# Kernel optimization log

Measured on AMD Instinct MI355X. Metric: run time of the kernel, lower is better.

The kernel has to match this reference:

```python
import jax, jax.numpy as jnp
import numpy as np

N_NODES = 100000
N_EDGES = 1600000
N_GRAPHS = 512
HIDDEN = 128
N_LAYERS = 3


def setup_inputs() -> dict:
    key = jax.random.key(0)
    ks = jax.random.split(key, 16)
    X = jax.random.normal(ks[0], (N_NODES, HIDDEN), dtype=jnp.float32)
    edge_index = jax.random.randint(ks[1], (2, N_EDGES), 0, N_NODES, dtype=jnp.int64)
    batch = jnp.sort(jax.random.randint(ks[2], (N_NODES,), 0, N_GRAPHS, dtype=jnp.int64))
    s = 1.0 / np.sqrt(HIDDEN)
    mlp_w1 = jax.random.normal(ks[3], (N_LAYERS, HIDDEN, HIDDEN), dtype=jnp.float32) * s
    mlp_b1 = jnp.zeros((N_LAYERS, HIDDEN), dtype=jnp.float32)
    mlp_w2 = jax.random.normal(ks[4], (N_LAYERS, HIDDEN, HIDDEN), dtype=jnp.float32) * s
    mlp_b2 = jnp.zeros((N_LAYERS, HIDDEN), dtype=jnp.float32)
    cls_w1 = jax.random.normal(ks[5], (HIDDEN * N_LAYERS, HIDDEN), dtype=jnp.float32) / np.sqrt(HIDDEN * N_LAYERS)
    cls_b1 = jnp.zeros((HIDDEN,), dtype=jnp.float32)
    cls_w2 = jax.random.normal(ks[6], (HIDDEN, HIDDEN), dtype=jnp.float32) * s
    cls_b2 = jnp.zeros((HIDDEN,), dtype=jnp.float32)
    cls_w3 = jax.random.normal(ks[7], (HIDDEN, 1), dtype=jnp.float32) * s
    cls_b3 = jnp.zeros((1,), dtype=jnp.float32)
    return {"X": X, "edge_index": edge_index, "batch": batch,
            "mlp_w1": mlp_w1, "mlp_b1": mlp_b1, "mlp_w2": mlp_w2, "mlp_b2": mlp_b2,
            "cls_w1": cls_w1, "cls_b1": cls_b1, "cls_w2": cls_w2, "cls_b2": cls_b2,
            "cls_w3": cls_w3, "cls_b3": cls_b3}


def reference(X, edge_index, batch, mlp_w1, mlp_b1, mlp_w2, mlp_b2,
              cls_w1, cls_b1, cls_w2, cls_b2, cls_w3, cls_b3):
    src, dst = edge_index[0], edge_index[1]
    xs = []
    for l in range(N_LAYERS):
        # GIN aggregation: sum_{j in N(i)} x_j ; eps = 0 so add self feature
        agg = jax.ops.segment_sum(X[src], dst, num_segments=N_NODES)  # [N, H]
        z = X + agg
        # 2-layer MLP update
        h = jax.nn.relu(z @ mlp_w1[l] + mlp_b1[l])
        h = h @ mlp_w2[l] + mlp_b2[l]
        # dropout is identity in eval; then relu
        X = jax.nn.relu(h)
        # global sum pooling per graph
        xs.append(jax.ops.segment_sum(X, batch, num_segments=N_GRAPHS))  # [G, H]
    h = jnp.concatenate(xs, axis=-1)  # JK 'cat' -> [G, H*L]
    h = jax.nn.relu(h @ cls_w1 + cls_b1)
    h = jax.nn.relu(h @ cls_w2 + cls_b2)
    logits = h @ cls_w3 + cls_b3  # [G, 1]
    return logits
```

## Files before the change

kernel.cpp:

```cpp
#include <hip/hip_runtime.h>
#include <hip/hip_fp16.h>
#include <cstddef>
#include <cstdint>

#define N_NODES   100000
#define N_EDGES   1600000
#define N_GRAPHS  512
#define HIDDEN    128
#define N_LAYERS  3

#define N_WIN        400
#define WIN_NODES    (N_NODES / N_WIN)
#define PLACE_BLOCKS 128
#define PCHUNK       (N_EDGES / PLACE_BLOCKS)

#define F2H_BLOCKS   ((N_NODES * HIDDEN / 8) / 256)
#define WCONV_BLOCKS (N_LAYERS * 2 * 16)
#define GB_BLOCKS    2
#define PREP_BLOCKS  (F2H_BLOCKS + WCONV_BLOCKS + GB_BLOCKS)

typedef _Float16 half8  __attribute__((ext_vector_type(8)));
typedef _Float16 half4v __attribute__((ext_vector_type(4)));
typedef _Float16 half2v __attribute__((ext_vector_type(2)));
typedef float    float8 __attribute__((ext_vector_type(8)));
typedef float    floatx4 __attribute__((ext_vector_type(4)));
typedef float    floatx2 __attribute__((ext_vector_type(2)));

__global__ __launch_bounds__(256) void win_count_kernel(const int* __restrict__ dst,
                                                        int* __restrict__ counts) {
    __shared__ int cs[N_WIN];
    for (int i = threadIdx.x; i < N_WIN; i += 256) cs[i] = 0;
    __syncthreads();
    const int4* d4 = (const int4*)(dst + blockIdx.x * PCHUNK);
    for (int i = threadIdx.x; i < PCHUNK / 4; i += 256) {
        int4 d = d4[i];
        atomicAdd(&cs[d.x / WIN_NODES], 1);
        atomicAdd(&cs[d.y / WIN_NODES], 1);
        atomicAdd(&cs[d.z / WIN_NODES], 1);
        atomicAdd(&cs[d.w / WIN_NODES], 1);
    }
    __syncthreads();
    for (int i = threadIdx.x; i < N_WIN; i += 256)
        counts[blockIdx.x * N_WIN + i] = cs[i];
}

__global__ __launch_bounds__(128) void win_scan1_kernel(const int* __restrict__ counts,
                                                        int* __restrict__ offsets,
                                                        int* __restrict__ colsum) {
    __shared__ int tmp[128];
    const int w = blockIdx.x;
    const int t = threadIdx.x;
    tmp[t] = counts[t * N_WIN + w];
    __syncthreads();
#pragma unroll
    for (int off = 1; off < 128; off <<= 1) {
        int u = (t >= off) ? tmp[t - off] : 0;
        __syncthreads();
        tmp[t] += u;
        __syncthreads();
    }
    offsets[t * N_WIN + w] = (t == 0) ? 0 : tmp[t - 1];
    if (t == 127) colsum[w] = tmp[127];
}

__global__ __launch_bounds__(512) void win_place_kernel(const int* __restrict__ src,
                                                        const int* __restrict__ dst,
                                                        const int* __restrict__ offsets,
                                                        const int* __restrict__ colsum,
                                                        int2* __restrict__ wedge) {
    __shared__ int ws[512];
    __shared__ int off[N_WIN];
    const int t = threadIdx.x;
    ws[t] = (t < N_WIN) ? colsum[t] : 0;
    __syncthreads();
#pragma unroll
    for (int o = 1; o < 512; o <<= 1) {
        int u = (t >= o) ? ws[t - o] : 0;
        __syncthreads();
        ws[t] += u;
        __syncthreads();
    }
    if (t < N_WIN) off[t] = offsets[blockIdx.x * N_WIN + t] + ((t == 0) ? 0 : ws[t - 1]);
    __syncthreads();
    const int4* d4 = (const int4*)(dst + blockIdx.x * PCHUNK);
    const int4* s4 = (const int4*)(src + blockIdx.x * PCHUNK);
    for (int i = t; i < PCHUNK / 4; i += 512) {
        int4 d = d4[i];
        int4 s = s4[i];
        int p0 = atomicAdd(&off[d.x / WIN_NODES], 1); wedge[p0] = make_int2(d.x, s.x);
        int p1 = atomicAdd(&off[d.y / WIN_NODES], 1); wedge[p1] = make_int2(d.y, s.y);
        int p2 = atomicAdd(&off[d.z / WIN_NODES], 1); wedge[p2] = make_int2(d.z, s.z);
        int p3 = atomicAdd(&off[d.w / WIN_NODES], 1); wedge[p3] = make_int2(d.w, s.w);
    }
}

__global__ __launch_bounds__(512) void win_csr_kernel(const int2* __restrict__ wedge,
                                                      const int* __restrict__ colsum,
                                                      int* __restrict__ row_ptr,
                                                      int* __restrict__ csr_src) {
    __shared__ int ws[512];
    __shared__ int cnt[WIN_NODES];
    __shared__ int bb[2];
    const int w = blockIdx.x, n0 = w * WIN_NODES, t = threadIdx.x;
    ws[t] = (t < N_WIN) ? colsum[t] : 0;
    __syncthreads();
#pragma unroll
    for (int o = 1; o < 512; o <<= 1) {
        int u = (t >= o) ? ws[t - o] : 0;
        __syncthreads();
        ws[t] += u;
        __syncthreads();
    }
    if (t == 0) { bb[0] = (w > 0) ? ws[w - 1] : 0; bb[1] = ws[w]; }
    if (w == N_WIN - 1 && t == 0) row_ptr[N_NODES] = ws[N_WIN - 1];
    for (int i = t; i < WIN_NODES; i += 512) cnt[i] = 0;
    __syncthreads();
    const int b0 = bb[0], b1 = bb[1];
    for (int e = b0 + t; e < b1; e += 512)
        atomicAdd(&cnt[wedge[e].x - n0], 1);
    __syncthreads();
    ws[t] = (t < WIN_NODES) ? cnt[t] : 0;
    __syncthreads();
#pragma unroll
    for (int o = 1; o < 512; o <<= 1) {
        int u = (t >= o) ? ws[t - o] : 0;
        __syncthreads();
        ws[t] += u;
        __syncthreads();
    }
    const int excl = (t == 0) ? 0 : ws[t - 1];
    if (t < WIN_NODES) {
        row_ptr[n0 + t] = b0 + excl;
        cnt[t] = b0 + excl;
    }
    __syncthreads();
    for (int e = b0 + t; e < b1; e += 512) {
        int2 ed = wedge[e];
        int p = atomicAdd(&cnt[ed.x - n0], 1);
        csr_src[p] = ed.y;
    }
}

__global__ __launch_bounds__(256) void prep_kernel(const float* __restrict__ X,
                                                   __half* __restrict__ hA,
                                                   unsigned char* __restrict__ outq,
                                                   const float* __restrict__ w1,
                                                   const float* __restrict__ w2,
                                                   __half* __restrict__ wt1,
                                                   __half* __restrict__ wt2,
                                                   const int* __restrict__ batch,
                                                   int* __restrict__ gstart) {
    __shared__ float tile[32][33];
    const int b = blockIdx.x;
    if (b < F2H_BLOCKS) {
        int t = b * 256 + threadIdx.x;
        const float4* in4 = (const float4*)X;
        float4 a = in4[t * 2 + 0];
        float4 c = in4[t * 2 + 1];
        __half2* o2 = (__half2*)hA;
        o2[t * 4 + 0] = __floats2half2_rn(a.x, a.y);
        o2[t * 4 + 1] = __floats2half2_rn(a.z, a.w);
        o2[t * 4 + 2] = __floats2half2_rn(c.x, c.y);
        o2[t * 4 + 3] = __floats2half2_rn(c.z, c.w);
        unsigned r0 = 0, r1 = 0;
        r0 = __builtin_amdgcn_cvt_pk_fp8_f32(a.x, a.y, r0, false);
        r0 = __builtin_amdgcn_cvt_pk_fp8_f32(a.z, a.w, r0, true);
        r1 = __builtin_amdgcn_cvt_pk_fp8_f32(c.x, c.y, r1, false);
        r1 = __builtin_amdgcn_cvt_pk_fp8_f32(c.z, c.w, r1, true);
        ((uint2*)outq)[t] = make_uint2(r0, r1);
    } else if (b < F2H_BLOCKS + WCONV_BLOCKS) {
        const int bb = b - F2H_BLOCKS;
        const int mat = bb & 1;
        const int tt = (bb >> 1) & 15;
        const int l  = bb >> 5;
        const int ti = (tt >> 2) * 32, tj = (tt & 3) * 32;
        const float* W = (mat ? w2 : w1) + (size_t)l * HIDDEN * HIDDEN;
        __half* WT = (mat ? wt2 : wt1) + (size_t)l * HIDDEN * HIDDEN;
        const int r = threadIdx.x >> 5;
        const int c = threadIdx.x & 31;
#pragma unroll
        for (int rr = 0; rr < 4; ++rr)
            tile[r + 8 * rr][c] = W[(size_t)(ti + r + 8 * rr) * HIDDEN + tj + c];
        __syncthreads();
#pragma unroll
        for (int rr = 0; rr < 4; ++rr)
            WT[(size_t)(tj + r + 8 * rr) * HIDDEN + ti + c] =
                __float2half(tile[c][r + 8 * rr]);
    } else {
        const int g = (b - F2H_BLOCKS - WCONV_BLOCKS) * 256 + threadIdx.x;
        if (g < N_GRAPHS) {
            int lo = 0, hi = N_NODES;
            while (lo < hi) {
                int mid = (lo + hi) >> 1;
                if (batch[mid] < g) lo = mid + 1; else hi = mid;
            }
            gstart[g] = lo;
        }
        if (g == 0) gstart[N_GRAPHS] = N_NODES;
    }
}

__device__ __forceinline__ void acc_fp8x16(float* acc, uint4 v) {
    floatx2 f;
    f = __builtin_amdgcn_cvt_pk_f32_fp8(v.x, false); acc[0] += f.x;  acc[1] += f.y;
    f = __builtin_amdgcn_cvt_pk_f32_fp8(v.x, true);  acc[2] += f.x;  acc[3] += f.y;
    f = __builtin_amdgcn_cvt_pk_f32_fp8(v.y, false); acc[4] += f.x;  acc[5] += f.y;
    f = __builtin_amdgcn_cvt_pk_f32_fp8(v.y, true);  acc[6] += f.x;  acc[7] += f.y;
    f = __builtin_amdgcn_cvt_pk_f32_fp8(v.z, false); acc[8] += f.x;  acc[9] += f.y;
    f = __builtin_amdgcn_cvt_pk_f32_fp8(v.z, true);  acc[10] += f.x; acc[11] += f.y;
    f = __builtin_amdgcn_cvt_pk_f32_fp8(v.w, false); acc[12] += f.x; acc[13] += f.y;
    f = __builtin_amdgcn_cvt_pk_f32_fp8(v.w, true);  acc[14] += f.x; acc[15] += f.y;
}

__global__ void gather_kernel(const unsigned char* __restrict__ Xq,
                              const __half* __restrict__ Xh,
                              __half* __restrict__ Zh,
                              const int* __restrict__ row_ptr,
                              const int* __restrict__ csr_src) {
    int wave = (blockIdx.x * blockDim.x + threadIdx.x) >> 6;
    int lane = threadIdx.x & 63;
    if (wave >= N_NODES) return;
    const int grp = lane >> 3;
    const int m   = lane & 7;
    const uint4* Q = (const uint4*)Xq;

    float acc[16];
#pragma unroll
    for (int j = 0; j < 16; ++j) acc[j] = 0.f;

    int k = row_ptr[wave];
    const int end = row_ptr[wave + 1];

    for (; k + 16 <= end; k += 16) {
        int n0 = csr_src[k + grp];
        int n1 = csr_src[k + 8 + grp];
        uint4 v0 = Q[(size_t)n0 * 8 + m];
        uint4 v1 = Q[(size_t)n1 * 8 + m];
        acc_fp8x16(acc, v0);
        acc_fp8x16(acc, v1);
    }
    if (k + 8 <= end) {
        int n0 = csr_src[k + grp];
        uint4 v0 = Q[(size_t)n0 * 8 + m];
        acc_fp8x16(acc, v0);
        k += 8;
    }
    int rem = end - k;
    if (grp < rem) {
        int n0 = csr_src[k + grp];
        uint4 v0 = Q[(size_t)n0 * 8 + m];
        acc_fp8x16(acc, v0);
    }

    half2v hh[8];
#pragma unroll
    for (int j = 0; j < 8; ++j) {
        hh[j][0] = (_Float16)acc[2 * j];
        hh[j][1] = (_Float16)acc[2 * j + 1];
    }
#pragma unroll
    for (int j = 0; j < 8; ++j) {
        int b = __shfl_xor(__builtin_bit_cast(int, hh[j]), 8);
        hh[j] = hh[j] + __builtin_bit_cast(half2v, b);
    }
#pragma unroll
    for (int j = 0; j < 8; ++j) {
        int b = __shfl_xor(__builtin_bit_cast(int, hh[j]), 16);
        hh[j] = hh[j] + __builtin_bit_cast(half2v, b);
    }
#pragma unroll
    for (int j = 0; j < 8; ++j) {
        int b = __shfl_xor(__builtin_bit_cast(int, hh[j]), 32);
        hh[j] = hh[j] + __builtin_bit_cast(half2v, b);
    }

    if (grp == 0) {
        const half2v* H2 = (const half2v*)(Xh + (size_t)wave * HIDDEN + 16 * m);
        half8 o0, o1;
#pragma unroll
        for (int j = 0; j < 4; ++j) {
            half2v s = hh[j] + H2[j];
            o0[2 * j] = s[0]; o0[2 * j + 1] = s[1];
        }
#pragma unroll
        for (int j = 0; j < 4; ++j) {
            half2v s = hh[4 + j] + H2[4 + j];
            o1[2 * j] = s[0]; o1[2 * j + 1] = s[1];
        }
        ((half8*)(Zh + (size_t)wave * HIDDEN + 16 * m))[0] = o0;
        ((half8*)(Zh + (size_t)wave * HIDDEN + 16 * m))[1] = o1;
    }
}

#define MM_BLOCKS 512
__global__ __launch_bounds__(256, 2) void mm_stage_kernel(const __half* __restrict__ A,
                                                          const __half* __restrict__ Wt,
                                                          const float* __restrict__ bias,
                                                          __half* __restrict__ C16,
                                                          unsigned char* __restrict__ Q8) {
    const int gwave = (blockIdx.x * 256 + threadIdx.x) >> 6;
    const int lane  = threadIdx.x & 63;
    const int m = lane & 15;
    const int q = lane >> 4;
    const int nwaves = MM_BLOCKS * 4;
    const int NTILES = N_NODES / 16;

    half8 wf[8][4];
    float bl[8][4];
#pragma unroll
    for (int ct = 0; ct < 8; ++ct) {
        const half8* Wrow = (const half8*)(Wt + (size_t)(ct * 16 + m) * HIDDEN);
#pragma unroll
        for (int c = 0; c < 4; ++c) wf[ct][c] = Wrow[c * 4 + q];
#pragma unroll
        for (int r = 0; r < 4; ++r) bl[ct][r] = bias[ct * 16 + q * 4 + r];
    }

    for (int t = gwave; t < NTILES; t += nwaves) {
        const half8* Arow = (const half8*)(A + (size_t)(t * 16 + m) * HIDDEN);
        half8 a0 = Arow[q];
        half8 a1 = Arow[4 + q];
        half8 a2 = Arow[8 + q];
        half8 a3 = Arow[12 + q];
        __half* Cr = C16 + (size_t)(t * 16 + m) * HIDDEN + q * 4;
#pragma unroll
        for (int ct = 0; ct < 8; ++ct) {
            floatx4 acc = {0.f, 0.f, 0.f, 0.f};
            acc = __builtin_amdgcn_mfma_f32_16x16x32_f16(wf[ct][0], a0, acc, 0, 0, 0);
            acc = __builtin_amdgcn_mfma_f32_16x16x32_f16(wf[ct][1], a1, acc, 0, 0, 0);
            acc = __builtin_amdgcn_mfma_f32_16x16x32_f16(wf[ct][2], a2, acc, 0, 0, 0);
            acc = __builtin_amdgcn_mfma_f32_16x16x32_f16(wf[ct][3], a3, acc, 0, 0, 0);
            float v0 = fmaxf(acc[0] + bl[ct][0], 0.f);
            float v1 = fmaxf(acc[1] + bl[ct][1], 0.f);
            float v2 = fmaxf(acc[2] + bl[ct][2], 0.f);
            float v3 = fmaxf(acc[3] + bl[ct][3], 0.f);
            half4v o;
            o[0] = (_Float16)v0; o[1] = (_Float16)v1;
            o[2] = (_Float16)v2; o[3] = (_Float16)v3;
            *(half4v*)(Cr + ct * 16) = o;
            if (Q8) {
                unsigned r0 = 0;
                r0 = __builtin_amdgcn_cvt_pk_fp8_f32(v0, v1, r0, false);
                r0 = __builtin_amdgcn_cvt_pk_fp8_f32(v2, v3, r0, true);
                *(unsigned*)(Q8 + (size_t)(t * 16 + m) * HIDDEN + ct * 16 + q * 4) = r0;
            }
        }
    }
}

__global__ __launch_bounds__(256) void gpool_kernel(const __half* __restrict__ Xh,
                                                    const int* __restrict__ gstart,
                                                    float* __restrict__ pooled,
                                                    int layer) {
    __shared__ float red[16][16][8];
    const int g  = blockIdx.x;
    const int f8 = threadIdx.x & 15;
    const int qt = threadIdx.x >> 4;
    const int s = gstart[g], e = gstart[g + 1];

    float acc[8];
#pragma unroll
    for (int j = 0; j < 8; ++j) acc[j] = 0.f;

    for (int n = s + qt; n < e; n += 16) {
        half8 v = ((const half8*)(Xh + (size_t)n * HIDDEN))[f8];
#pragma unroll
        for (int j = 0; j < 8; ++j) acc[j] += (float)v[j];
    }
#pragma unroll
    for (int j = 0; j < 8; ++j) red[qt][f8][j] = acc[j];
    __syncthreads();

    if (threadIdx.x < 128) {
        const int c = threadIdx.x;
        float sum = 0.f;
#pragma unroll
        for (int p = 0; p < 16; ++p) sum += red[p][c >> 3][c & 7];
        pooled[(size_t)g * (HIDDEN * N_LAYERS) + layer * HIDDEN + c] = sum;
    }
}

__global__ __launch_bounds__(128) void cls_kernel(const float* __restrict__ pooled,
                                                  const float* __restrict__ w1,
                                                  const float* __restrict__ b1,
                                                  const float* __restrict__ w2,
                                                  const float* __restrict__ b2,
                                                  const float* __restrict__ w3,
                                                  const float* __restrict__ b3,
                                                  float* __restrict__ out) {
    __shared__ float hin[HIDDEN * N_LAYERS];
    __shared__ float h1[HIDDEN];
    __shared__ float red[HIDDEN];
    const int g = blockIdx.x;
    const int t = threadIdx.x;

    for (int i = t; i < HIDDEN * N_LAYERS; i += 128)
        hin[i] = pooled[(size_t)g * (HIDDEN * N_LAYERS) + i];
    __syncthreads();

    float s = 0.f;
    for (int k = 0; k < HIDDEN * N_LAYERS; ++k) s += hin[k] * w1[(size_t)k * HIDDEN + t];
    s = fmaxf(s + b1[t], 0.f);
    h1[t] = s;
    __syncthreads();

    float s2 = 0.f;
    for (int k = 0; k < HIDDEN; ++k) s2 += h1[k] * w2[(size_t)k * HIDDEN + t];
    s2 = fmaxf(s2 + b2[t], 0.f);

    red[t] = s2 * w3[t];
    __syncthreads();
    for (int off = 64; off > 0; off >>= 1) {
        if (t < off) red[t] += red[t + off];
        __syncthreads();
    }
    if (t == 0) out[g] = red[0] + b3[0];
}

extern "C" void kernel_launch(void* const* d_in, const int* in_sizes, int n_in,
                              void* d_out, int out_size, void* d_ws, size_t ws_size,
                              hipStream_t stream) {
    const float* X     = (const float*)d_in[0];
    const int*   ei    = (const int*)d_in[1];
    const int*   batch = (const int*)d_in[2];
    const float* w1all = (const float*)d_in[3];
    const float* b1all = (const float*)d_in[4];
    const float* w2all = (const float*)d_in[5];
    const float* b2all = (const float*)d_in[6];
    const float* cw1   = (const float*)d_in[7];
    const float* cb1   = (const float*)d_in[8];
    const float* cw2   = (const float*)d_in[9];
    const float* cb2   = (const float*)d_in[10];
    const float* cw3   = (const float*)d_in[11];
    const float* cb3   = (const float*)d_in[12];
    float* out = (float*)d_out;

    const int* src = ei;
    const int* dst = ei + N_EDGES;

    char* p = (char*)d_ws;
    auto alloc2 = [&](size_t bytes) {
        char* r = p;
        p += (bytes + 255) & ~(size_t)255;
        return r;
    };
    __half* hA      = (__half*)alloc2((size_t)N_NODES * HIDDEN * sizeof(__half));
    __half* hB      = (__half*)alloc2((size_t)N_NODES * HIDDEN * sizeof(__half));
    __half* zh      = (__half*)alloc2((size_t)N_NODES * HIDDEN * sizeof(__half));
    __half* m1h     = (__half*)alloc2((size_t)N_NODES * HIDDEN * sizeof(__half));
    unsigned char* qbuf = (unsigned char*)alloc2((size_t)N_NODES * HIDDEN);
    __half* wt1     = (__half*)alloc2((size_t)N_LAYERS * HIDDEN * HIDDEN * sizeof(__half));
    __half* wt2     = (__half*)alloc2((size_t)N_LAYERS * HIDDEN * HIDDEN * sizeof(__half));
    int2*   wedge   = (int2*)alloc2((size_t)N_EDGES * sizeof(int2));
    int*    csr     = (int*)alloc2((size_t)N_EDGES * sizeof(int));
    int*    rowp    = (int*)alloc2((size_t)(N_NODES + 1) * sizeof(int));
    int*    counts  = (int*)alloc2((size_t)PLACE_BLOCKS * N_WIN * sizeof(int));
    int*    offsets = (int*)alloc2((size_t)PLACE_BLOCKS * N_WIN * sizeof(int));
    int*    colsum  = (int*)alloc2((size_t)N_WIN * sizeof(int));
    int*    gstart  = (int*)alloc2((size_t)(N_GRAPHS + 1) * sizeof(int));
    float*  pooled  = (float*)alloc2((size_t)N_GRAPHS * HIDDEN * N_LAYERS * sizeof(float));

    win_count_kernel<<<PLACE_BLOCKS, 256, 0, stream>>>(dst, counts);
    win_scan1_kernel<<<N_WIN, 128, 0, stream>>>(counts, offsets, colsum);
    win_place_kernel<<<PLACE_BLOCKS, 512, 0, stream>>>(src, dst, offsets, colsum, wedge);
    win_csr_kernel<<<N_WIN, 512, 0, stream>>>(wedge, colsum, rowp, csr);

    prep_kernel<<<PREP_BLOCKS, 256, 0, stream>>>(X, hA, qbuf, w1all, w2all, wt1, wt2,
                                                 batch, gstart);

    const int gat_grid = (N_NODES + 3) / 4;

    __half* hcur = hA;
    for (int l = 0; l < N_LAYERS; ++l) {
        __half* hnext = (l & 1) ? hA : hB;
        const bool emit = (l < N_LAYERS - 1);
        gather_kernel<<<gat_grid, 256, 0, stream>>>(qbuf, hcur, zh, rowp, csr);
        mm_stage_kernel<<<MM_BLOCKS, 256, 0, stream>>>(zh,
                                                       wt1 + (size_t)l * HIDDEN * HIDDEN,
                                                       b1all + (size_t)l * HIDDEN,
                                                       m1h, (unsigned char*)nullptr);
        mm_stage_kernel<<<MM_BLOCKS, 256, 0, stream>>>(m1h,
                                                       wt2 + (size_t)l * HIDDEN * HIDDEN,
                                                       b2all + (size_t)l * HIDDEN,
                                                       hnext,
                                                       emit ? qbuf : (unsigned char*)nullptr);
        gpool_kernel<<<N_GRAPHS, 256, 0, stream>>>(hnext, gstart, pooled, l);
        hcur = hnext;
    }

    cls_kernel<<<N_GRAPHS, 128, 0, stream>>>(pooled, cw1, cb1, cw2, cb2, cw3, cb3, out);
}
```

Before: 456.2 us.

## Fuse both MLP matmuls into one kernel and merge pooling into next gather

Replaces the two separate MFMA stage kernels per layer with a single kernel that keeps the hidden activation in registers, moving it between the two matmuls by lane shuffles instead of writing and re-reading an fp16 intermediate buffer. Both weight matrices are staged in XOR-swizzled shared memory, and the next tile's A rows are prefetched. Graph pooling of the previous layer now runs as extra blocks inside the following gather launch, which cuts kernel launches. In exchange the fused kernel uses 64KB of shared memory per block, which may limit occupancy, and the shuffle-based fragment relayout adds cross-lane traffic.

```diff
diff --git a/kernel.cpp b/kernel.cpp
--- a/kernel.cpp
+++ b/kernel.cpp
@@ -212,14 +212,12 @@
     f = __builtin_amdgcn_cvt_pk_f32_fp8(v.w, true);  acc[14] += f.x; acc[15] += f.y;
 }
 
-__global__ void gather_kernel(const unsigned char* __restrict__ Xq,
-                              const __half* __restrict__ Xh,
-                              __half* __restrict__ Zh,
-                              const int* __restrict__ row_ptr,
-                              const int* __restrict__ csr_src) {
-    int wave = (blockIdx.x * blockDim.x + threadIdx.x) >> 6;
-    int lane = threadIdx.x & 63;
-    if (wave >= N_NODES) return;
+__device__ __forceinline__ void gather_body(int wave, int lane,
+                                            const unsigned char* __restrict__ Xq,
+                                            const __half* __restrict__ Xh,
+                                            __half* __restrict__ Zh,
+                                            const int* __restrict__ row_ptr,
+                                            const int* __restrict__ csr_src) {
     const int grp = lane >> 3;
     const int m   = lane & 7;
     const uint4* Q = (const uint4*)Xq;
@@ -292,48 +290,184 @@
     }
 }
 
+__global__ void gather_kernel(const unsigned char* __restrict__ Xq,
+                              const __half* __restrict__ Xh,
+                              __half* __restrict__ Zh,
+                              const int* __restrict__ row_ptr,
+                              const int* __restrict__ csr_src) {
+    int wave = (blockIdx.x * blockDim.x + threadIdx.x) >> 6;
+    if (wave >= N_NODES) return;
+    gather_body(wave, threadIdx.x & 63, Xq, Xh, Zh, row_ptr, csr_src);
+}
+
+__device__ __forceinline__ void gpool_body(int g,
+                                           const __half* __restrict__ Xh,
+                                           const int* __restrict__ gstart,
+                                           float* __restrict__ pooled, int layer) {
+    __shared__ float red[16][16][8];
+    const int f8 = threadIdx.x & 15;
+    const int qt = threadIdx.x >> 4;
+    const int s = gstart[g], e = gstart[g + 1];
+
+    float acc[8];
+#pragma unroll
+    for (int j = 0; j < 8; ++j) acc[j] = 0.f;
+
+    for (int n = s + qt; n < e; n += 16) {
+        half8 v = ((const half8*)(Xh + (size_t)n * HIDDEN))[f8];
+#pragma unroll
+        for (int j = 0; j < 8; ++j) acc[j] += (float)v[j];
+    }
+#pragma unroll
+    for (int j = 0; j < 8; ++j) red[qt][f8][j] = acc[j];
+    __syncthreads();
+
+    if (threadIdx.x < 128) {
+        const int c = threadIdx.x;
+        float sum = 0.f;
+#pragma unroll
+        for (int p = 0; p < 16; ++p) sum += red[p][c >> 3][c & 7];
+        pooled[(size_t)g * (HIDDEN * N_LAYERS) + layer * HIDDEN + c] = sum;
+    }
+}
+
+__global__ __launch_bounds__(256) void gpool_kernel(const __half* __restrict__ Xh,
+                                                    const int* __restrict__ gstart,
+                                                    float* __restrict__ pooled,
+                                                    int layer) {
+    gpool_body(blockIdx.x, Xh, gstart, pooled, layer);
+}
+
+#define POOL_BLKS N_GRAPHS
+__global__ __launch_bounds__(256) void gather_pool_kernel(const unsigned char* __restrict__ Xq,
+                                                          const __half* __restrict__ Xh,
+                                                          __half* __restrict__ Zh,
+                                                          const int* __restrict__ row_ptr,
+                                                          const int* __restrict__ csr_src,
+                                                          const int* __restrict__ gstart,
+                                                          float* __restrict__ pooled,
+                                                          int prev_layer) {
+    if (blockIdx.x < POOL_BLKS) {
+        gpool_body(blockIdx.x, Xh, gstart, pooled, prev_layer);
+        return;
+    }
+    int wave = ((blockIdx.x - POOL_BLKS) * 256 + threadIdx.x) >> 6;
+    if (wave >= N_NODES) return;
+    gather_body(wave, threadIdx.x & 63, Xq, Xh, Zh, row_ptr, csr_src);
+}
+
 #define MM_BLOCKS 512
-__global__ __launch_bounds__(256, 2) void mm_stage_kernel(const __half* __restrict__ A,
-                                                          const __half* __restrict__ Wt,
-                                                          const float* __restrict__ bias,
-                                                          __half* __restrict__ C16,
-                                                          unsigned char* __restrict__ Q8) {
-    const int gwave = (blockIdx.x * 256 + threadIdx.x) >> 6;
-    const int lane  = threadIdx.x & 63;
-    const int m = lane & 15;
-    const int q = lane >> 4;
+__global__ __launch_bounds__(256, 2) void mlp2_kernel(const __half* __restrict__ A,
+                                                      const __half* __restrict__ Wt1,
+                                                      const __half* __restrict__ Wt2,
+                                                      const float* __restrict__ b1,
+                                                      const float* __restrict__ b2,
+                                                      __half* __restrict__ C16,
+                                                      unsigned char* __restrict__ Q8) {
+    __shared__ __half w1s[128][128];
+    __shared__ __half w2s[128][128];
+
+    const int tid  = threadIdx.x;
+    const int lane = tid & 63;
+    const int m    = lane & 15;
+    const int q    = lane >> 4;
+
+    {
+        const half8* s1 = (const half8*)Wt1;
+        const half8* s2 = (const half8*)Wt2;
+        for (int j = tid; j < 128 * 16; j += 256) {
+            int r  = j >> 4;
+            int cs = (j & 15) ^ (r & 15);
+            *(half8*)&w1s[r][cs * 8] = s1[j];
+            *(half8*)&w2s[r][cs * 8] = s2[j];
+        }
+    }
+
+    float bl1[8][4], bl2[8][4];
+#pragma unroll
+    for (int ct = 0; ct < 8; ++ct)
+#pragma unroll
+        for (int r = 0; r < 4; ++r) {
+            bl1[ct][r] = b1[ct * 16 + q * 4 + r];
+            bl2[ct][r] = b2[ct * 16 + q * 4 + r];
+        }
+    __syncthreads();
+
+    const int gwave  = (blockIdx.x * 256 + tid) >> 6;
     const int nwaves = MM_BLOCKS * 4;
     const int NTILES = N_NODES / 16;
 
-    half8 wf[8][4];
-    float bl[8][4];
-#pragma unroll
-    for (int ct = 0; ct < 8; ++ct) {
-        const half8* Wrow = (const half8*)(Wt + (size_t)(ct * 16 + m) * HIDDEN);
-#pragma unroll
-        for (int c = 0; c < 4; ++c) wf[ct][c] = Wrow[c * 4 + q];
-#pragma unroll
-        for (int r = 0; r < 4; ++r) bl[ct][r] = bias[ct * 16 + q * 4 + r];
-    }
-
-    for (int t = gwave; t < NTILES; t += nwaves) {
+    const int src0 = m + ((lane & 16) << 1);
+    const int src1 = src0 + 16;
+    const bool sel = ((lane >> 5) & 1) != 0;
+
+    if (gwave >= NTILES) return;
+
+    int t = gwave;
+    half8 a0, a1, a2, a3;
+    {
         const half8* Arow = (const half8*)(A + (size_t)(t * 16 + m) * HIDDEN);
-        half8 a0 = Arow[q];
-        half8 a1 = Arow[4 + q];
-        half8 a2 = Arow[8 + q];
-        half8 a3 = Arow[12 + q];
+        a0 = Arow[q]; a1 = Arow[4 + q]; a2 = Arow[8 + q]; a3 = Arow[12 + q];
+    }
+
+    while (true) {
+        const int tn = t + nwaves;
+        half8 n0, n1, n2, n3;
+        if (tn < NTILES) {
+            const half8* Nrow = (const half8*)(A + (size_t)(tn * 16 + m) * HIDDEN);
+            n0 = Nrow[q]; n1 = Nrow[4 + q]; n2 = Nrow[8 + q]; n3 = Nrow[12 + q];
+        }
+
+        uint2 hh[8];
+#pragma unroll
+        for (int ct = 0; ct < 8; ++ct) {
+            const _Float16* wrow = (const _Float16*)&w1s[ct * 16 + m][0];
+            floatx4 acc = {0.f, 0.f, 0.f, 0.f};
+            acc = __builtin_amdgcn_mfma_f32_16x16x32_f16(*(const half8*)(wrow + (((0 + q) ^ m) * 8)),  a0, acc, 0, 0, 0);
+            acc = __builtin_amdgcn_mfma_f32_16x16x32_f16(*(const half8*)(wrow + (((4 + q) ^ m) * 8)),  a1, acc, 0, 0, 0);
+            acc = __builtin_amdgcn_mfma_f32_16x16x32_f16(*(const half8*)(wrow + (((8 + q) ^ m) * 8)),  a2, acc, 0, 0, 0);
+            acc = __builtin_amdgcn_mfma_f32_16x16x32_f16(*(const half8*)(wrow + (((12 + q) ^ m) * 8)), a3, acc, 0, 0, 0);
+            half2v p0, p1;
+            p0[0] = (_Float16)fmaxf(acc[0] + bl1[ct][0], 0.f);
+            p0[1] = (_Float16)fmaxf(acc[1] + bl1[ct][1], 0.f);
+            p1[0] = (_Float16)fmaxf(acc[2] + bl1[ct][2], 0.f);
+            p1[1] = (_Float16)fmaxf(acc[3] + bl1[ct][3], 0.f);
+            hh[ct].x = __builtin_bit_cast(unsigned, p0);
+            hh[ct].y = __builtin_bit_cast(unsigned, p1);
+        }
+
+        half8 hf[4];
+#pragma unroll
+        for (int c = 0; c < 4; ++c) {
+            unsigned ax = (unsigned)__shfl((int)hh[2 * c].x,     src0);
+            unsigned ay = (unsigned)__shfl((int)hh[2 * c].y,     src0);
+            unsigned az = (unsigned)__shfl((int)hh[2 * c].x,     src1);
+            unsigned aw = (unsigned)__shfl((int)hh[2 * c].y,     src1);
+            unsigned bx = (unsigned)__shfl((int)hh[2 * c + 1].x, src0);
+            unsigned by = (unsigned)__shfl((int)hh[2 * c + 1].y, src0);
+            unsigned bz = (unsigned)__shfl((int)hh[2 * c + 1].x, src1);
+            unsigned bw = (unsigned)__shfl((int)hh[2 * c + 1].y, src1);
+            uint4 u;
+            u.x = sel ? bx : ax;
+            u.y = sel ? by : ay;
+            u.z = sel ? bz : az;
+            u.w = sel ? bw : aw;
+            hf[c] = __builtin_bit_cast(half8, u);
+        }
+
         __half* Cr = C16 + (size_t)(t * 16 + m) * HIDDEN + q * 4;
 #pragma unroll
         for (int ct = 0; ct < 8; ++ct) {
+            const _Float16* wrow = (const _Float16*)&w2s[ct * 16 + m][0];
             floatx4 acc = {0.f, 0.f, 0.f, 0.f};
-            acc = __builtin_amdgcn_mfma_f32_16x16x32_f16(wf[ct][0], a0, acc, 0, 0, 0);
-            acc = __builtin_amdgcn_mfma_f32_16x16x32_f16(wf[ct][1], a1, acc, 0, 0, 0);
-            acc = __builtin_amdgcn_mfma_f32_16x16x32_f16(wf[ct][2], a2, acc, 0, 0, 0);
-            acc = __builtin_amdgcn_mfma_f32_16x16x32_f16(wf[ct][3], a3, acc, 0, 0, 0);
-            float v0 = fmaxf(acc[0] + bl[ct][0], 0.f);
-            float v1 = fmaxf(acc[1] + bl[ct][1], 0.f);
-            float v2 = fmaxf(acc[2] + bl[ct][2], 0.f);
-            float v3 = fmaxf(acc[3] + bl[ct][3], 0.f);
+            acc = __builtin_amdgcn_mfma_f32_16x16x32_f16(*(const half8*)(wrow + (((0 + q) ^ m) * 8)),  hf[0], acc, 0, 0, 0);
+            acc = __builtin_amdgcn_mfma_f32_16x16x32_f16(*(const half8*)(wrow + (((4 + q) ^ m) * 8)),  hf[1], acc, 0, 0, 0);
+            acc = __builtin_amdgcn_mfma_f32_16x16x32_f16(*(const half8*)(wrow + (((8 + q) ^ m) * 8)),  hf[2], acc, 0, 0, 0);
+            acc = __builtin_amdgcn_mfma_f32_16x16x32_f16(*(const half8*)(wrow + (((12 + q) ^ m) * 8)), hf[3], acc, 0, 0, 0);
+            float v0 = fmaxf(acc[0] + bl2[ct][0], 0.f);
+            float v1 = fmaxf(acc[1] + bl2[ct][1], 0.f);
+            float v2 = fmaxf(acc[2] + bl2[ct][2], 0.f);
+            float v3 = fmaxf(acc[3] + bl2[ct][3], 0.f);
             half4v o;
             o[0] = (_Float16)v0; o[1] = (_Float16)v1;
             o[2] = (_Float16)v2; o[3] = (_Float16)v3;
@@ -345,38 +479,10 @@
                 *(unsigned*)(Q8 + (size_t)(t * 16 + m) * HIDDEN + ct * 16 + q * 4) = r0;
             }
         }
-    }
-}
-
-__global__ __launch_bounds__(256) void gpool_kernel(const __half* __restrict__ Xh,
-                                                    const int* __restrict__ gstart,
-                                                    float* __restrict__ pooled,
-                                                    int layer) {
-    __shared__ float red[16][16][8];
-    const int g  = blockIdx.x;
-    const int f8 = threadIdx.x & 15;
-    const int qt = threadIdx.x >> 4;
-    const int s = gstart[g], e = gstart[g + 1];
-
-    float acc[8];
-#pragma unroll
-    for (int j = 0; j < 8; ++j) acc[j] = 0.f;
-
-    for (int n = s + qt; n < e; n += 16) {
-        half8 v = ((const half8*)(Xh + (size_t)n * HIDDEN))[f8];
-#pragma unroll
-        for (int j = 0; j < 8; ++j) acc[j] += (float)v[j];
-    }
-#pragma unroll
-    for (int j = 0; j < 8; ++j) red[qt][f8][j] = acc[j];
-    __syncthreads();
-
-    if (threadIdx.x < 128) {
-        const int c = threadIdx.x;
-        float sum = 0.f;
-#pragma unroll
-        for (int p = 0; p < 16; ++p) sum += red[p][c >> 3][c & 7];
-        pooled[(size_t)g * (HIDDEN * N_LAYERS) + layer * HIDDEN + c] = sum;
+
+        if (tn >= NTILES) break;
+        t = tn;
+        a0 = n0; a1 = n1; a2 = n2; a3 = n3;
     }
 }
 
@@ -447,7 +553,6 @@
     __half* hA      = (__half*)alloc2((size_t)N_NODES * HIDDEN * sizeof(__half));
     __half* hB      = (__half*)alloc2((size_t)N_NODES * HIDDEN * sizeof(__half));
     __half* zh      = (__half*)alloc2((size_t)N_NODES * HIDDEN * sizeof(__half));
-    __half* m1h     = (__half*)alloc2((size_t)N_NODES * HIDDEN * sizeof(__half));
     unsigned char* qbuf = (unsigned char*)alloc2((size_t)N_NODES * HIDDEN);
     __half* wt1     = (__half*)alloc2((size_t)N_LAYERS * HIDDEN * HIDDEN * sizeof(__half));
     __half* wt2     = (__half*)alloc2((size_t)N_LAYERS * HIDDEN * HIDDEN * sizeof(__half));
@@ -474,19 +579,22 @@
     for (int l = 0; l < N_LAYERS; ++l) {
         __half* hnext = (l & 1) ? hA : hB;
         const bool emit = (l < N_LAYERS - 1);
-        gather_kernel<<<gat_grid, 256, 0, stream>>>(qbuf, hcur, zh, rowp, csr);
-        mm_stage_kernel<<<MM_BLOCKS, 256, 0, stream>>>(zh,
-                                                       wt1 + (size_t)l * HIDDEN * HIDDEN,
-                                                       b1all + (size_t)l * HIDDEN,
-                                                       m1h, (unsigned char*)nullptr);
-        mm_stage_kernel<<<MM_BLOCKS, 256, 0, stream>>>(m1h,
-                                                       wt2 + (size_t)l * HIDDEN * HIDDEN,
-                                                       b2all + (size_t)l * HIDDEN,
-                                                       hnext,
-                                                       emit ? qbuf : (unsigned char*)nullptr);
-        gpool_kernel<<<N_GRAPHS, 256, 0, stream>>>(hnext, gstart, pooled, l);
+        if (l == 0) {
+            gather_kernel<<<gat_grid, 256, 0, stream>>>(qbuf, hcur, zh, rowp, csr);
+        } else {
+            gather_pool_kernel<<<gat_grid + POOL_BLKS, 256, 0, stream>>>(
+                qbuf, hcur, zh, rowp, csr, gstart, pooled, l - 1);
+        }
+        mlp2_kernel<<<MM_BLOCKS, 256, 0, stream>>>(zh,
+                                                   wt1 + (size_t)l * HIDDEN * HIDDEN,
+                                                   wt2 + (size_t)l * HIDDEN * HIDDEN,
+                                                   b1all + (size_t)l * HIDDEN,
+                                                   b2all + (size_t)l * HIDDEN,
+                                                   hnext,
+                                                   emit ? qbuf : (unsigned char*)nullptr);
         hcur = hnext;
     }
 
+    gpool_kernel<<<N_GRAPHS, 256, 0, stream>>>(hcur, gstart, pooled, N_LAYERS - 1);
     cls_kernel<<<N_GRAPHS, 128, 0, stream>>>(pooled, cw1, cb1, cw2, cb2, cw3, cb3, out);
 }
```

Result: slower. 517.5 us (+13.4%).
